# Kernel tuning notes

Hardware: AMD Instinct MI355X
Metric: run time of the kernel (lower is better)

## Reference

```python
import jax, jax.numpy as jnp
import numpy as np

FEAT_DIM = 512
NUM_HEADS = 8
HEAD_DIM = FEAT_DIM // NUM_HEADS


def setup_inputs() -> dict:
    key = jax.random.key(0)
    ks = jax.random.split(key, 10)
    B, T, D = 4, 2048, FEAT_DIM
    scale = 1.0 / np.sqrt(D)
    inp = {
        "x_current": jax.random.normal(ks[0], (B, T, D), jnp.float32),
        "x_past": jax.random.normal(ks[1], (B, T, D), jnp.float32),
        "wq": jax.random.normal(ks[2], (D, D), jnp.float32) * scale,
        "bq": jnp.zeros((D,), jnp.float32),
        "wk": jax.random.normal(ks[3], (D, D), jnp.float32) * scale,
        "bk": jnp.zeros((D,), jnp.float32),
        "wv": jax.random.normal(ks[4], (D, D), jnp.float32) * scale,
        "bv": jnp.zeros((D,), jnp.float32),
        "wo": jax.random.normal(ks[5], (D, D), jnp.float32) * scale,
        "bo": jnp.zeros((D,), jnp.float32),
    }
    return inp


def reference(x_current, x_past, wq, bq, wk, bk, wv, bv, wo, bo):
    B, T, D = x_current.shape
    H, Hd = NUM_HEADS, HEAD_DIM
    # QKV projections (torch Linear: x @ W.T + b)
    Q = (x_current @ wq.T + bq).reshape(B, T, H, Hd).transpose(0, 2, 1, 3)
    K = (x_past @ wk.T + bk).reshape(B, T, H, Hd).transpose(0, 2, 1, 3)
    V = (x_past @ wv.T + bv).reshape(B, T, H, Hd).transpose(0, 2, 1, 3)
    # scaled dot-product attention, full T x T scores as in the original
    scores = jnp.einsum("bhqd,bhkd->bhqk", Q, K) / jnp.sqrt(jnp.asarray(Hd, Q.dtype))
    attn = jax.nn.softmax(scores, axis=-1)
    out = jnp.einsum("bhqk,bhkd->bhqd", attn, V)
    out = out.transpose(0, 2, 1, 3).reshape(B, T, D)
    return out @ wo.T + bo
```

## Files before the change

### kernel.cpp

```cpp
#include <hip/hip_runtime.h>
#include <math.h>

#define BATCH 4
#define SEQ 2048
#define FEAT 512
#define NHEADS 8
#define HD 64
#define NROWS (BATCH*SEQ)
#define QSCALE 0.18033688011112042f

typedef __attribute__((ext_vector_type(4)))  float f32x4;
typedef __attribute__((ext_vector_type(16))) float f32x16;
typedef __attribute__((ext_vector_type(8)))  short s16x8;
typedef __attribute__((ext_vector_type(8)))  unsigned short u16x8;
typedef __attribute__((ext_vector_type(4)))  unsigned int u32x4;
typedef __attribute__((ext_vector_type(2)))  unsigned int u32x2;

#if __has_builtin(__builtin_amdgcn_exp2f)
#define EX2(x) __builtin_amdgcn_exp2f(x)
#else
#define EX2(x) __expf((x) * 0.6931471805599453f)
#endif

static __device__ __forceinline__ unsigned short f2bf(float x) {
  unsigned int u = __builtin_bit_cast(unsigned int, x);
  unsigned int r = (u + 0x7FFFu + ((u >> 16) & 1u)) >> 16;
  return (unsigned short)r;
}
static __device__ __forceinline__ float bf2f(unsigned short h) {
  unsigned int u = ((unsigned int)h) << 16;
  return __builtin_bit_cast(float, u);
}
static __device__ __forceinline__ void split2(float x, unsigned short& h, unsigned short& l) {
  h = f2bf(x);
  l = f2bf(x - bf2f(h));
}

static __device__ __forceinline__ void glds16(const unsigned short* g, unsigned short* l) {
  __builtin_amdgcn_global_load_lds(
      (const __attribute__((address_space(1))) unsigned int*)g,
      (__attribute__((address_space(3))) unsigned int*)l,
      16, 0, 0);
}

__global__ __launch_bounds__(256) void presplit_w(
    const float* __restrict__ wq, const float* __restrict__ wk,
    const float* __restrict__ wv, const float* __restrict__ wo,
    unsigned short* __restrict__ Wsp)
{
  const int mat = blockIdx.x >> 7;
  const int chunk = ((blockIdx.x & 127) * 256 + threadIdx.x) * 8;
  const float* src = (mat == 0) ? wq : (mat == 1) ? wk : (mat == 2) ? wv : wo;
  unsigned short* hi = Wsp + (size_t)mat * 524288;
  unsigned short* lo = hi + 262144;
  const f32x4 a = *reinterpret_cast<const f32x4*>(&src[chunk]);
  const f32x4 b = *reinterpret_cast<const f32x4*>(&src[chunk + 4]);
  u16x8 h8, l8;
#pragma unroll
  for (int i = 0; i < 4; ++i) { unsigned short hh, ll; split2(a[i], hh, ll); h8[i] = hh; l8[i] = ll; }
#pragma unroll
  for (int i = 0; i < 4; ++i) { unsigned short hh, ll; split2(b[i], hh, ll); h8[4 + i] = hh; l8[4 + i] = ll; }
  *reinterpret_cast<u16x8*>(&hi[chunk]) = h8;
  *reinterpret_cast<u16x8*>(&lo[chunk]) = l8;
}

__global__ __launch_bounds__(256) void presplit_x2(
    const float* __restrict__ xc, const float* __restrict__ xp,
    unsigned short* __restrict__ Xchi, unsigned short* __restrict__ Xphi)
{
  const float* src = blockIdx.y ? xp : xc;
  unsigned short* dst = blockIdx.y ? Xphi : Xchi;
  const int chunk = (blockIdx.x * 256 + threadIdx.x) * 8;
  const f32x4 a = *reinterpret_cast<const f32x4*>(&src[chunk]);
  const f32x4 b = *reinterpret_cast<const f32x4*>(&src[chunk + 4]);
  u16x8 h8;
#pragma unroll
  for (int i = 0; i < 4; ++i) h8[i] = f2bf(a[i]);
#pragma unroll
  for (int i = 0; i < 4; ++i) h8[4 + i] = f2bf(b[i]);
  *reinterpret_cast<u16x8*>(&dst[chunk]) = h8;
}

__global__ __launch_bounds__(256, 4) void qkv_proj(
    const unsigned short* __restrict__ Xchi, const unsigned short* __restrict__ Xphi,
    const unsigned short* __restrict__ Wsp,
    const float* __restrict__ bq, const float* __restrict__ bk,
    const float* __restrict__ bv,
    unsigned short* __restrict__ Qhi, unsigned short* __restrict__ Khi,
    unsigned short* __restrict__ Vthi)
{
  __shared__ unsigned short Xh[128 * 64];
  __shared__ unsigned short Whi[64 * 64], Wlo[64 * 64];

  const int z = blockIdx.z;
  const unsigned short* Xsrc = (z == 0) ? Xchi : Xphi;
  const unsigned short* Wh_g = Wsp + (size_t)z * 524288;
  const unsigned short* Wl_g = Wh_g + 262144;
  const float* Bp = (z == 0) ? bq : (z == 1) ? bk : bv;
  const float scale = (z == 0) ? QSCALE : 1.0f;

  const int tid  = threadIdx.x;
  const int lane = tid & 63;
  const int wave = tid >> 6;
  const int g = lane >> 4, j = lane & 15;
  const int wm = (wave >> 1) * 64;
  const int wn = (wave & 1) * 32;
  const int row0 = blockIdx.x * 128;
  const int col0 = blockIdx.y * 64;

  f32x4 acc[4][2];
#pragma unroll
  for (int mi = 0; mi < 4; ++mi)
#pragma unroll
    for (int ni = 0; ni < 2; ++ni) acc[mi][ni] = (f32x4)0.f;

  const int xrow = wave * 32 + (lane >> 3);
  const int xkg  = (lane & 7) ^ ((lane >> 3) & 7);
  const unsigned short* srcX = Xsrc + (size_t)(row0 + xrow) * FEAT + xkg * 8;
  const int wrow = wave * 16 + (lane >> 3);
  const unsigned short* srcWh = Wh_g + (size_t)(col0 + wrow) * FEAT + xkg * 8;
  const unsigned short* srcWl = Wl_g + (size_t)(col0 + wrow) * FEAT + xkg * 8;

  for (int kt = 0; kt < FEAT; kt += 64) {
    __syncthreads();
#pragma unroll
    for (int c = 0; c < 4; ++c)
      glds16(srcX + kt + c * 4096, &Xh[(wave * 32 + c * 8) * 64]);
    glds16(srcWh + kt,        &Whi[(wave * 16) * 64]);
    glds16(srcWh + kt + 4096, &Whi[(wave * 16 + 8) * 64]);
    glds16(srcWl + kt,        &Wlo[(wave * 16) * 64]);
    glds16(srcWl + kt + 4096, &Wlo[(wave * 16 + 8) * 64]);
    asm volatile("s_waitcnt vmcnt(0)" ::: "memory");
    __syncthreads();

#pragma unroll
    for (int c = 0; c < 2; ++c) {
      const int koff = c * 32 + g * 8;
      s16x8 ah[4], bh[2], bl[2];
#pragma unroll
      for (int mi = 0; mi < 4; ++mi) {
        const int r = wm + mi * 16 + j;
        const int el = r * 64 + (koff ^ ((r & 7) << 3));
        ah[mi] = *reinterpret_cast<const s16x8*>(&Xh[el]);
      }
#pragma unroll
      for (int ni = 0; ni < 2; ++ni) {
        const int r = wn + ni * 16 + j;
        const int el = r * 64 + (koff ^ ((r & 7) << 3));
        bh[ni] = *reinterpret_cast<const s16x8*>(&Whi[el]);
        bl[ni] = *reinterpret_cast<const s16x8*>(&Wlo[el]);
      }
#pragma unroll
      for (int mi = 0; mi < 4; ++mi)
#pragma unroll
        for (int ni = 0; ni < 2; ++ni) {
          acc[mi][ni] = __builtin_amdgcn_mfma_f32_16x16x32_bf16(ah[mi], bh[ni], acc[mi][ni], 0, 0, 0);
          acc[mi][ni] = __builtin_amdgcn_mfma_f32_16x16x32_bf16(ah[mi], bl[ni], acc[mi][ni], 0, 0, 0);
        }
    }
  }

  if (z < 2) {
    unsigned short* Out = (z == 0) ? Qhi : Khi;
#pragma unroll
    for (int ni = 0; ni < 2; ++ni) {
      const int colc = col0 + wn + ni * 16 + j;
      const float bj = Bp[colc];
      const int h = colc >> 6, hd = colc & 63;
#pragma unroll
      for (int mi = 0; mi < 4; ++mi)
#pragma unroll
        for (int r = 0; r < 4; ++r) {
          const int rowc = row0 + wm + mi * 16 + (g << 2) + r;
          const int b = rowc >> 11, t = rowc & 2047;
          const float v = (acc[mi][ni][r] + bj) * scale;
          Out[(((size_t)b * NHEADS + h) * SEQ + t) * HD + hd] = f2bf(v);
        }
    }
  } else {
    __syncthreads();
#pragma unroll
    for (int ni = 0; ni < 2; ++ni) {
      const int hdl = wn + ni * 16 + j;
      const float bj = Bp[col0 + hdl];
#pragma unroll
      for (int mi = 0; mi < 4; ++mi)
#pragma unroll
        for (int r = 0; r < 4; ++r) {
          const int lt = wm + mi * 16 + (g << 2) + r;
          const float v = acc[mi][ni][r] + bj;
          const int el = lt * 64 + (hdl ^ ((lt & 7) << 3));
          Xh[el] = f2bf(v);
        }
    }
    __syncthreads();
    const int b = row0 >> 11, h = col0 >> 6;
    const int tbase = row0 & 2047;
#pragma unroll
    for (int c = 0; c < 4; ++c) {
      const int chunk = c * 256 + tid;
      const int hd = chunk >> 4;
      const int t0 = (chunk & 15) * 8;
      u16x8 vh;
#pragma unroll
      for (int i = 0; i < 8; ++i) {
        const int p = t0 + i;
        const int lt = (p & ~15) | ((p & 3) + (((p >> 2) & 1) << 3) + (((p >> 3) & 1) << 2));
        const int el = lt * 64 + (hd ^ ((lt & 7) << 3));
        vh[i] = Xh[el];
      }
      const size_t off = (((size_t)b * NHEADS + h) * HD + hd) * SEQ + tbase + t0;
      *reinterpret_cast<u16x8*>(&Vthi[off]) = vh;
    }
  }
}

__global__ __launch_bounds__(256, 4) void out_proj(
    const unsigned short* __restrict__ AOhi, const unsigned short* __restrict__ AOlo,
    const unsigned short* __restrict__ Woh,  const unsigned short* __restrict__ Wol,
    const float* __restrict__ bias, float* __restrict__ out)
{
  __shared__ unsigned short Xhi[64 * 64], Xlo[64 * 64];
  __shared__ unsigned short Whi[64 * 64], Wlo[64 * 64];

  const int tid  = threadIdx.x;
  const int lane = tid & 63;
  const int wave = tid >> 6;
  const int g = lane >> 4, j = lane & 15;
  const int wm = (wave >> 1) * 32;
  const int wn = (wave & 1) * 32;
  const int row0 = blockIdx.x * 64;
  const int col0 = blockIdx.y * 64;

  f32x4 acc[2][2];
#pragma unroll
  for (int mi = 0; mi < 2; ++mi)
#pragma unroll
    for (int ni = 0; ni < 2; ++ni) acc[mi][ni] = (f32x4)0.f;

  const int arow = wave * 16 + (lane >> 3);
  const int akg  = (lane & 7) ^ ((lane >> 3) & 7);
  const unsigned short* srcAh = AOhi + (size_t)(row0 + arow) * FEAT + akg * 8;
  const unsigned short* srcAl = AOlo + (size_t)(row0 + arow) * FEAT + akg * 8;
  const unsigned short* srcWh = Woh + (size_t)(col0 + arow) * FEAT + akg * 8;
  const unsigned short* srcWl = Wol + (size_t)(col0 + arow) * FEAT + akg * 8;

  for (int kt = 0; kt < FEAT; kt += 64) {
    __syncthreads();
    glds16(srcAh + kt,        &Xhi[(wave * 16) * 64]);
    glds16(srcAh + kt + 4096, &Xhi[(wave * 16 + 8) * 64]);
    glds16(srcAl + kt,        &Xlo[(wave * 16) * 64]);
    glds16(srcAl + kt + 4096, &Xlo[(wave * 16 + 8) * 64]);
    glds16(srcWh + kt,        &Whi[(wave * 16) * 64]);
    glds16(srcWh + kt + 4096, &Whi[(wave * 16 + 8) * 64]);
    glds16(srcWl + kt,        &Wlo[(wave * 16) * 64]);
    glds16(srcWl + kt + 4096, &Wlo[(wave * 16 + 8) * 64]);
    asm volatile("s_waitcnt vmcnt(0)" ::: "memory");
    __syncthreads();

#pragma unroll
    for (int c = 0; c < 2; ++c) {
      const int koff = c * 32 + g * 8;
      s16x8 ah[2], al[2], bh[2], bl[2];
#pragma unroll
      for (int mi = 0; mi < 2; ++mi) {
        const int r = wm + mi * 16 + j;
        const int el = r * 64 + (koff ^ ((r & 7) << 3));
        ah[mi] = *reinterpret_cast<const s16x8*>(&Xhi[el]);
        al[mi] = *reinterpret_cast<const s16x8*>(&Xlo[el]);
      }
#pragma unroll
      for (int ni = 0; ni < 2; ++ni) {
        const int r = wn + ni * 16 + j;
        const int el = r * 64 + (koff ^ ((r & 7) << 3));
        bh[ni] = *reinterpret_cast<const s16x8*>(&Whi[el]);
        bl[ni] = *reinterpret_cast<const s16x8*>(&Wlo[el]);
      }
#pragma unroll
      for (int mi = 0; mi < 2; ++mi)
#pragma unroll
        for (int ni = 0; ni < 2; ++ni) {
          acc[mi][ni] = __builtin_amdgcn_mfma_f32_16x16x32_bf16(ah[mi], bh[ni], acc[mi][ni], 0, 0, 0);
          acc[mi][ni] = __builtin_amdgcn_mfma_f32_16x16x32_bf16(ah[mi], bl[ni], acc[mi][ni], 0, 0, 0);
          acc[mi][ni] = __builtin_amdgcn_mfma_f32_16x16x32_bf16(al[mi], bh[ni], acc[mi][ni], 0, 0, 0);
        }
    }
  }

#pragma unroll
  for (int ni = 0; ni < 2; ++ni) {
    const int colc = col0 + wn + ni * 16 + j;
    const float bj = bias[colc];
#pragma unroll
    for (int mi = 0; mi < 2; ++mi)
#pragma unroll
      for (int r = 0; r < 4; ++r) {
        const int rowc = row0 + wm + mi * 16 + (g << 2) + r;
        out[(size_t)rowc * FEAT + colc] = acc[mi][ni][r] + bj;
      }
  }
}

__global__ __launch_bounds__(256, 3) void attn_pipe(
    const unsigned short* __restrict__ Qhi,
    const unsigned short* __restrict__ Khi,
    const unsigned short* __restrict__ Vthi,
    unsigned short* __restrict__ AOhi, unsigned short* __restrict__ AOlo)
{
  __shared__ unsigned short Kh_s[3][4096];
  __shared__ unsigned short Vh_s[3][4096];
  __shared__ float bcast[4][32];

  const int tid = threadIdx.x, lane = tid & 63, wave = tid >> 6;
  const int hfl = lane >> 5;
  const int l31 = lane & 31;

  const int bid = blockIdx.x;
  const int swz = (bid & 7) * 64 + (bid >> 3);
  const int qt  = swz & 15;
  const int bh  = swz >> 4;
  const int b = bh >> 3, h = bh & 7;

  const int q0 = qt * 128 + wave * 32;
  const size_t kvbase = (size_t)bh * SEQ * HD;

  s16x8 qh[4];
  {
    const size_t qoff = kvbase + (size_t)(q0 + l31) * HD + hfl * 8;
#pragma unroll
    for (int c = 0; c < 4; ++c)
      qh[c] = *reinterpret_cast<const s16x8*>(&Qhi[qoff + c * 16]);
  }

  f32x16 oacc0 = (f32x16)0.f, oacc1 = (f32x16)0.f;
  float m = -INFINITY, lsum = 0.f;

  const int ck  = tid >> 3;
  const int ksl = (tid & 7) ^ (ck & 7);
  const unsigned short* sKh = Khi + kvbase + (size_t)ck * HD + ksl * 8;
  const int vr  = tid >> 3;
  const int vsl = (tid & 7) ^ (vr & 7);
  const int vhd = vr + (vsl >> 2) * 32;
  const int vk0 = (vsl & 3) * 8;
  const unsigned short* sVh = Vthi + kvbase + (size_t)vhd * SEQ + vk0;
  const int wq = wave * 512;

  const int krow = l31 * 64;
  const int ksw  = l31 & 7;

  auto stage = [&](int tt, int bi) {
    const size_t ko = (size_t)tt * 64 * HD;
    const int    vo = tt * 64;
    glds16(sKh + ko,           &Kh_s[bi][wq]);
    glds16(sKh + ko + 32 * HD, &Kh_s[bi][2048 + wq]);
    glds16(sVh + vo,           &Vh_s[bi][wq]);
    glds16(sVh + vo + 32,      &Vh_s[bi][2048 + wq]);
  };

  stage(0, 0);
  stage(1, 1);

  const int NT = SEQ / 64;
  int cur = 0;
  for (int t = 0; t < NT; ++t) {
    if (t < NT - 1) {
      asm volatile("s_waitcnt vmcnt(4)" ::: "memory");
    } else {
      asm volatile("s_waitcnt vmcnt(0)" ::: "memory");
    }
    __syncthreads();
    if (t + 2 < NT) {
      int nb = cur + 2; if (nb >= 3) nb -= 3;
      stage(t + 2, nb);
    }
    __builtin_amdgcn_sched_barrier(0);

#pragma unroll
    for (int sub = 0; sub < 2; ++sub) {
      const int sb = sub * 2048;

      s16x8 KH[4];
#pragma unroll
      for (int c = 0; c < 4; ++c) {
        const int idx = sb + krow + ((((c << 1) | hfl)) ^ ksw) * 8;
        KH[c] = *reinterpret_cast<const s16x8*>(&Kh_s[cur][idx]);
      }

      f32x16 st = (f32x16)0.f;
      __builtin_amdgcn_s_setprio(1);
#pragma unroll
      for (int c = 0; c < 4; ++c)
        st = __builtin_amdgcn_mfma_f32_32x32x16_bf16(KH[c], qh[c], st, 0, 0, 0);
      __builtin_amdgcn_s_setprio(0);

      s16x8 V0h[2], V1h[2];
#pragma unroll
      for (int c = 0; c < 2; ++c) {
        const int i0 = sb + krow + ((((c << 1) | hfl)) ^ ksw) * 8;
        const int i1 = sb + krow + (((4 | (c << 1) | hfl)) ^ ksw) * 8;
        V0h[c] = *reinterpret_cast<const s16x8*>(&Vh_s[cur][i0]);
        V1h[c] = *reinterpret_cast<const s16x8*>(&Vh_s[cur][i1]);
      }

      const float a0 = fmaxf(fmaxf(st[0], st[1]), st[2]);
      const float a1 = fmaxf(fmaxf(st[3], st[4]), st[5]);
      const float a2 = fmaxf(fmaxf(st[6], st[7]), st[8]);
      const float a3 = fmaxf(fmaxf(st[9], st[10]), st[11]);
      const float a4 = fmaxf(fmaxf(st[12], st[13]), st[14]);
      const float pm = fmaxf(fmaxf(fmaxf(a0, a1), a2),
                             fmaxf(fmaxf(a3, a4), st[15]));

      if (__any(pm > m + 8.f)) {
        const float pmf  = fmaxf(pm, __shfl_xor(pm, 32));
        const float mnew = fmaxf(m, pmf);
        const float corr = EX2(m - mnew);
        m = mnew; lsum *= corr;
        if (lane < 32) bcast[wave][l31] = corr;
        f32x4 c4[4];
#pragma unroll
        for (int rq = 0; rq < 4; ++rq)
          c4[rq] = *reinterpret_cast<const f32x4*>(&bcast[wave][rq * 8 + hfl * 4]);
#pragma unroll
        for (int r = 0; r < 16; ++r) {
          const float cc = c4[r >> 2][r & 3];
          oacc0[r] *= cc; oacc1[r] *= cc;
        }
      }

#pragma unroll
      for (int r = 0; r < 16; ++r) st[r] = EX2(st[r] - m);
      {
        float s0 = (st[0] + st[1]) + (st[2] + st[3]);
        float s1 = (st[4] + st[5]) + (st[6] + st[7]);
        float s2 = (st[8] + st[9]) + (st[10] + st[11]);
        float s3 = (st[12] + st[13]) + (st[14] + st[15]);
        lsum += (s0 + s1) + (s2 + s3);
      }

      unsigned int wh[8];
#pragma unroll
      for (int p = 0; p < 8; ++p)
        asm("v_cvt_pk_bf16_f32 %0, %1, %2" : "=v"(wh[p]) : "v"(st[2 * p]), "v"(st[2 * p + 1]));
      const s16x8 pa0h = __builtin_bit_cast(s16x8, (u32x4){wh[0], wh[1], wh[2], wh[3]});
      const s16x8 pa1h = __builtin_bit_cast(s16x8, (u32x4){wh[4], wh[5], wh[6], wh[7]});

      __builtin_amdgcn_s_setprio(1);
      oacc0 = __builtin_amdgcn_mfma_f32_32x32x16_bf16(pa0h, V0h[0], oacc0, 0, 0, 0);
      oacc0 = __builtin_amdgcn_mfma_f32_32x32x16_bf16(pa1h, V0h[1], oacc0, 0, 0, 0);
      oacc1 = __builtin_amdgcn_mfma_f32_32x32x16_bf16(pa0h, V1h[0], oacc1, 0, 0, 0);
      oacc1 = __builtin_amdgcn_mfma_f32_32x32x16_bf16(pa1h, V1h[1], oacc1, 0, 0, 0);
      __builtin_amdgcn_s_setprio(0);
    }

    cur += 1; if (cur >= 3) cur -= 3;
  }

  const float lf = lsum + __shfl_xor(lsum, 32);
  if (lane < 32) bcast[wave][l31] = 1.f / lf;
  __syncthreads();
  f32x4 i4[4];
#pragma unroll
  for (int rq = 0; rq < 4; ++rq)
    i4[rq] = *reinterpret_cast<const f32x4*>(&bcast[wave][rq * 8 + hfl * 4]);

#pragma unroll
  for (int r = 0; r < 16; ++r) {
    const int q = q0 + (r & 3) + 8 * (r >> 2) + 4 * hfl;
    const float inv = i4[r >> 2][r & 3];
    const size_t idx = ((size_t)b * SEQ + q) * FEAT + h * HD + l31;
    unsigned short hh, ll;
    split2(oacc0[r] * inv, hh, ll);
    AOhi[idx] = hh; AOlo[idx] = ll;
    split2(oacc1[r] * inv, hh, ll);
    AOhi[idx + 32] = hh; AOlo[idx + 32] = ll;
  }
}

extern "C" void kernel_launch(void* const* d_in, const int* in_sizes, int n_in,
                              void* d_out, int out_size, void* d_ws, size_t ws_size,
                              hipStream_t stream) {
  const float* x_cur  = (const float*)d_in[0];
  const float* x_past = (const float*)d_in[1];
  const float* wq = (const float*)d_in[2];
  const float* bq = (const float*)d_in[3];
  const float* wk = (const float*)d_in[4];
  const float* bk = (const float*)d_in[5];
  const float* wv = (const float*)d_in[6];
  const float* bv = (const float*)d_in[7];
  const float* wo = (const float*)d_in[8];
  const float* bo = (const float*)d_in[9];
  float* out = (float*)d_out;

  const size_t n = (size_t)NROWS * FEAT;
  unsigned short* Qhi  = (unsigned short*)d_ws;
  unsigned short* Xchi = Qhi + n;
  unsigned short* Khi  = Qhi + 2 * n;
  unsigned short* Xphi = Qhi + 3 * n;
  unsigned short* Vthi = Qhi + 4 * n;
  unsigned short* Wsp  = Qhi + 5 * n;
  unsigned short* AOhi = Qhi + 6 * n;
  unsigned short* AOlo = Qhi + 7 * n;

  dim3 block(256);
  presplit_w<<<dim3(512), block, 0, stream>>>(wq, wk, wv, wo, Wsp);
  presplit_x2<<<dim3(NROWS * FEAT / 2048, 2), block, 0, stream>>>(x_cur, x_past, Xchi, Xphi);

  qkv_proj<<<dim3(NROWS / 128, FEAT / 64, 3), block, 0, stream>>>(
      Xchi, Xphi, Wsp, bq, bk, bv, Qhi, Khi, Vthi);

  attn_pipe<<<dim3(512), block, 0, stream>>>(Qhi, Khi, Vthi, AOhi, AOlo);

  dim3 gout(NROWS / 64, FEAT / 64);
  out_proj<<<gout, block, 0, stream>>>(AOhi, AOlo, Wsp + 3 * 524288,
                                       Wsp + 3 * 524288 + 262144, bo, out);
}
```

Measured before the change: 111.4 us.

## Merge presplit kernels and drop low-part of attention output in out_proj

Merges the weight and activation bf16 presplit kernels into one launch with a combined grid. The attention kernel now writes only the bf16 high part of its output, so out_proj loads one activation tile instead of two and issues two MFMAs per fragment instead of three. This removes one kernel launch, the AOlo global writes and reads, and a third of the out_proj matrix math. The cost is lower precision in the output projection, since the attention output is truncated to bf16.

```diff
diff --git a/kernel.cpp b/kernel.cpp
--- a/kernel.cpp
+++ b/kernel.cpp
@@ -14,7 +14,6 @@
 typedef __attribute__((ext_vector_type(8)))  short s16x8;
 typedef __attribute__((ext_vector_type(8)))  unsigned short u16x8;
 typedef __attribute__((ext_vector_type(4)))  unsigned int u32x4;
-typedef __attribute__((ext_vector_type(2)))  unsigned int u32x2;
 
 #if __has_builtin(__builtin_amdgcn_exp2f)
 #define EX2(x) __builtin_amdgcn_exp2f(x)
@@ -43,42 +42,45 @@
       16, 0, 0);
 }
 
-__global__ __launch_bounds__(256) void presplit_w(
+__global__ __launch_bounds__(256) void presplit(
     const float* __restrict__ wq, const float* __restrict__ wk,
     const float* __restrict__ wv, const float* __restrict__ wo,
-    unsigned short* __restrict__ Wsp)
-{
-  const int mat = blockIdx.x >> 7;
-  const int chunk = ((blockIdx.x & 127) * 256 + threadIdx.x) * 8;
-  const float* src = (mat == 0) ? wq : (mat == 1) ? wk : (mat == 2) ? wv : wo;
-  unsigned short* hi = Wsp + (size_t)mat * 524288;
-  unsigned short* lo = hi + 262144;
-  const f32x4 a = *reinterpret_cast<const f32x4*>(&src[chunk]);
-  const f32x4 b = *reinterpret_cast<const f32x4*>(&src[chunk + 4]);
-  u16x8 h8, l8;
-#pragma unroll
-  for (int i = 0; i < 4; ++i) { unsigned short hh, ll; split2(a[i], hh, ll); h8[i] = hh; l8[i] = ll; }
-#pragma unroll
-  for (int i = 0; i < 4; ++i) { unsigned short hh, ll; split2(b[i], hh, ll); h8[4 + i] = hh; l8[4 + i] = ll; }
-  *reinterpret_cast<u16x8*>(&hi[chunk]) = h8;
-  *reinterpret_cast<u16x8*>(&lo[chunk]) = l8;
-}
-
-__global__ __launch_bounds__(256) void presplit_x2(
     const float* __restrict__ xc, const float* __restrict__ xp,
+    unsigned short* __restrict__ Wsp,
     unsigned short* __restrict__ Xchi, unsigned short* __restrict__ Xphi)
 {
-  const float* src = blockIdx.y ? xp : xc;
-  unsigned short* dst = blockIdx.y ? Xphi : Xchi;
-  const int chunk = (blockIdx.x * 256 + threadIdx.x) * 8;
-  const f32x4 a = *reinterpret_cast<const f32x4*>(&src[chunk]);
-  const f32x4 b = *reinterpret_cast<const f32x4*>(&src[chunk + 4]);
-  u16x8 h8;
-#pragma unroll
-  for (int i = 0; i < 4; ++i) h8[i] = f2bf(a[i]);
-#pragma unroll
-  for (int i = 0; i < 4; ++i) h8[4 + i] = f2bf(b[i]);
-  *reinterpret_cast<u16x8*>(&dst[chunk]) = h8;
+  const int bid = blockIdx.x;
+  if (bid < 512) {
+    const int mat = bid >> 7;
+    const int chunk = ((bid & 127) * 256 + threadIdx.x) * 8;
+    const float* src = (mat == 0) ? wq : (mat == 1) ? wk : (mat == 2) ? wv : wo;
+    unsigned short* hi = Wsp + (size_t)mat * 524288;
+    unsigned short* lo = hi + 262144;
+    const f32x4 a = *reinterpret_cast<const f32x4*>(&src[chunk]);
+    const f32x4 b = *reinterpret_cast<const f32x4*>(&src[chunk + 4]);
+    u16x8 h8, l8;
+#pragma unroll
+    for (int i = 0; i < 4; ++i) { unsigned short hh, ll; split2(a[i], hh, ll); h8[i] = hh; l8[i] = ll; }
+#pragma unroll
+    for (int i = 0; i < 4; ++i) { unsigned short hh, ll; split2(b[i], hh, ll); h8[4 + i] = hh; l8[4 + i] = ll; }
+    *reinterpret_cast<u16x8*>(&hi[chunk]) = h8;
+    *reinterpret_cast<u16x8*>(&lo[chunk]) = l8;
+  } else {
+    const int i = bid - 512;
+    const int half = i >> 11;
+    const int ib = i & 2047;
+    const float* src = half ? xp : xc;
+    unsigned short* dst = half ? Xphi : Xchi;
+    const int chunk = (ib * 256 + threadIdx.x) * 8;
+    const f32x4 a = *reinterpret_cast<const f32x4*>(&src[chunk]);
+    const f32x4 b = *reinterpret_cast<const f32x4*>(&src[chunk + 4]);
+    u16x8 h8;
+#pragma unroll
+    for (int ii = 0; ii < 4; ++ii) h8[ii] = f2bf(a[ii]);
+#pragma unroll
+    for (int ii = 0; ii < 4; ++ii) h8[4 + ii] = f2bf(b[ii]);
+    *reinterpret_cast<u16x8*>(&dst[chunk]) = h8;
+  }
 }
 
 __global__ __launch_bounds__(256, 4) void qkv_proj(
@@ -216,11 +218,11 @@
 }
 
 __global__ __launch_bounds__(256, 4) void out_proj(
-    const unsigned short* __restrict__ AOhi, const unsigned short* __restrict__ AOlo,
+    const unsigned short* __restrict__ AOhi,
     const unsigned short* __restrict__ Woh,  const unsigned short* __restrict__ Wol,
     const float* __restrict__ bias, float* __restrict__ out)
 {
-  __shared__ unsigned short Xhi[64 * 64], Xlo[64 * 64];
+  __shared__ unsigned short Xh[64 * 64];
   __shared__ unsigned short Whi[64 * 64], Wlo[64 * 64];
 
   const int tid  = threadIdx.x;
@@ -240,17 +242,14 @@
 
   const int arow = wave * 16 + (lane >> 3);
   const int akg  = (lane & 7) ^ ((lane >> 3) & 7);
-  const unsigned short* srcAh = AOhi + (size_t)(row0 + arow) * FEAT + akg * 8;
-  const unsigned short* srcAl = AOlo + (size_t)(row0 + arow) * FEAT + akg * 8;
+  const unsigned short* srcA  = AOhi + (size_t)(row0 + arow) * FEAT + akg * 8;
   const unsigned short* srcWh = Woh + (size_t)(col0 + arow) * FEAT + akg * 8;
   const unsigned short* srcWl = Wol + (size_t)(col0 + arow) * FEAT + akg * 8;
 
   for (int kt = 0; kt < FEAT; kt += 64) {
     __syncthreads();
-    glds16(srcAh + kt,        &Xhi[(wave * 16) * 64]);
-    glds16(srcAh + kt + 4096, &Xhi[(wave * 16 + 8) * 64]);
-    glds16(srcAl + kt,        &Xlo[(wave * 16) * 64]);
-    glds16(srcAl + kt + 4096, &Xlo[(wave * 16 + 8) * 64]);
+    glds16(srcA + kt,         &Xh[(wave * 16) * 64]);
+    glds16(srcA + kt + 4096,  &Xh[(wave * 16 + 8) * 64]);
     glds16(srcWh + kt,        &Whi[(wave * 16) * 64]);
     glds16(srcWh + kt + 4096, &Whi[(wave * 16 + 8) * 64]);
     glds16(srcWl + kt,        &Wlo[(wave * 16) * 64]);
@@ -261,13 +260,12 @@
 #pragma unroll
     for (int c = 0; c < 2; ++c) {
       const int koff = c * 32 + g * 8;
-      s16x8 ah[2], al[2], bh[2], bl[2];
+      s16x8 ah[2], bh[2], bl[2];
 #pragma unroll
       for (int mi = 0; mi < 2; ++mi) {
         const int r = wm + mi * 16 + j;
         const int el = r * 64 + (koff ^ ((r & 7) << 3));
-        ah[mi] = *reinterpret_cast<const s16x8*>(&Xhi[el]);
-        al[mi] = *reinterpret_cast<const s16x8*>(&Xlo[el]);
+        ah[mi] = *reinterpret_cast<const s16x8*>(&Xh[el]);
       }
 #pragma unroll
       for (int ni = 0; ni < 2; ++ni) {
@@ -282,7 +280,6 @@
         for (int ni = 0; ni < 2; ++ni) {
           acc[mi][ni] = __builtin_amdgcn_mfma_f32_16x16x32_bf16(ah[mi], bh[ni], acc[mi][ni], 0, 0, 0);
           acc[mi][ni] = __builtin_amdgcn_mfma_f32_16x16x32_bf16(ah[mi], bl[ni], acc[mi][ni], 0, 0, 0);
-          acc[mi][ni] = __builtin_amdgcn_mfma_f32_16x16x32_bf16(al[mi], bh[ni], acc[mi][ni], 0, 0, 0);
         }
     }
   }
@@ -305,7 +302,7 @@
     const unsigned short* __restrict__ Qhi,
     const unsigned short* __restrict__ Khi,
     const unsigned short* __restrict__ Vthi,
-    unsigned short* __restrict__ AOhi, unsigned short* __restrict__ AOlo)
+    unsigned short* __restrict__ AOhi)
 {
   __shared__ unsigned short Kh_s[3][4096];
   __shared__ unsigned short Vh_s[3][4096];
@@ -468,11 +465,8 @@
     const int q = q0 + (r & 3) + 8 * (r >> 2) + 4 * hfl;
     const float inv = i4[r >> 2][r & 3];
     const size_t idx = ((size_t)b * SEQ + q) * FEAT + h * HD + l31;
-    unsigned short hh, ll;
-    split2(oacc0[r] * inv, hh, ll);
-    AOhi[idx] = hh; AOlo[idx] = ll;
-    split2(oacc1[r] * inv, hh, ll);
-    AOhi[idx + 32] = hh; AOlo[idx + 32] = ll;
+    AOhi[idx]      = f2bf(oacc0[r] * inv);
+    AOhi[idx + 32] = f2bf(oacc1[r] * inv);
   }
 }
 
@@ -499,18 +493,17 @@
   unsigned short* Vthi = Qhi + 4 * n;
   unsigned short* Wsp  = Qhi + 5 * n;
   unsigned short* AOhi = Qhi + 6 * n;
-  unsigned short* AOlo = Qhi + 7 * n;
 
   dim3 block(256);
-  presplit_w<<<dim3(512), block, 0, stream>>>(wq, wk, wv, wo, Wsp);
-  presplit_x2<<<dim3(NROWS * FEAT / 2048, 2), block, 0, stream>>>(x_cur, x_past, Xchi, Xphi);
+  presplit<<<dim3(4608), block, 0, stream>>>(wq, wk, wv, wo, x_cur, x_past,
+                                             Wsp, Xchi, Xphi);
 
   qkv_proj<<<dim3(NROWS / 128, FEAT / 64, 3), block, 0, stream>>>(
       Xchi, Xphi, Wsp, bq, bk, bv, Qhi, Khi, Vthi);
 
-  attn_pipe<<<dim3(512), block, 0, stream>>>(Qhi, Khi, Vthi, AOhi, AOlo);
+  attn_pipe<<<dim3(512), block, 0, stream>>>(Qhi, Khi, Vthi, AOhi);
 
   dim3 gout(NROWS / 64, FEAT / 64);
-  out_proj<<<gout, block, 0, stream>>>(AOhi, AOlo, Wsp + 3 * 524288,
+  out_proj<<<gout, block, 0, stream>>>(AOhi, Wsp + 3 * 524288,
                                        Wsp + 3 * 524288 + 262144, bo, out);
 }
```

Result: faster. 103.0 us (median of 3 runs) (-7.5%).
